# Performance work log

Measured on AMD Instinct MI355X. Metric: run time of the kernel, lower is better.

The kernel has to match this reference:

```python
import jax, jax.numpy as jnp
import numpy as np

N, E, D = 20000, 320000, 256
EPS = 1e-5


def setup_inputs() -> dict:
    key = jax.random.key(0)
    ks = jax.random.split(key, 12)
    s = 1.0 / np.sqrt(D)
    s2 = 1.0 / np.sqrt(2 * D)
    return {
        "node_embeddings": jax.random.normal(ks[0], (N, D), jnp.float32),
        "edge_index": jax.random.randint(ks[1], (2, E), 0, N, jnp.int64),
        "edge_embeddings": jax.random.normal(ks[2], (E, D), jnp.float32),
        # message MLP: Linear(D,D) -> GELU -> Linear(D,D)
        "W1m": jax.random.uniform(ks[3], (D, D), jnp.float32, -s, s),
        "b1m": jnp.zeros((D,), jnp.float32),
        "W2m": jax.random.uniform(ks[4], (D, D), jnp.float32, -s, s),
        "b2m": jnp.zeros((D,), jnp.float32),
        # update MLP: Linear(D,2D) -> GELU -> Linear(2D,D)
        "W1u": jax.random.uniform(ks[5], (D, 2 * D), jnp.float32, -s, s),
        "b1u": jnp.zeros((2 * D,), jnp.float32),
        "W2u": jax.random.uniform(ks[6], (2 * D, D), jnp.float32, -s2, s2),
        "b2u": jnp.zeros((D,), jnp.float32),
        # LayerNorm params
        "gamma": jnp.ones((D,), jnp.float32),
        "beta": jnp.zeros((D,), jnp.float32),
    }


def _layer_norm(x, gamma, beta):
    mu = jnp.mean(x, axis=-1, keepdims=True)
    var = jnp.mean(jnp.square(x - mu), axis=-1, keepdims=True)
    return (x - mu) * jax.lax.rsqrt(var + EPS) * gamma + beta


def reference(node_embeddings, edge_index, edge_embeddings,
              W1m, b1m, W2m, b2m, W1u, b1u, W2u, b2u, gamma, beta):
    src = edge_index[0]
    dst = edge_index[1]
    n = node_embeddings.shape[0]
    # gather + edge add + message MLP (exact erf GELU, as torch default)
    h = node_embeddings[src] + edge_embeddings           # [E, D]
    h = jax.nn.gelu(h @ W1m + b1m, approximate=False)
    messages = h @ W2m + b2m                             # [E, D]
    # scatter-mean aggregation
    agg = jax.ops.segment_sum(messages, dst, num_segments=n)  # [N, D]
    deg = jax.ops.segment_sum(jnp.ones((dst.shape[0], 1), node_embeddings.dtype),
                              dst, num_segments=n)            # [N, 1]
    agg = agg / jnp.maximum(deg, 1.0)
    # update MLP + residual + LayerNorm
    u = jax.nn.gelu(agg @ W1u + b1u, approximate=False) @ W2u + b2u
    return _layer_norm(node_embeddings + u, gamma, beta)
```

## Files before the change

kernel.cpp:

```cpp
#include <hip/hip_runtime.h>
#include <hip/hip_bf16.h>

#define N_NODES 20000
#define N_EDGES 320000
#define EBLK 64
#define NBLK 32

typedef __attribute__((ext_vector_type(8))) short short8;
typedef __attribute__((ext_vector_type(4))) float f32x4;

static __device__ __forceinline__ unsigned short f2bf(float f) {
  __hip_bfloat16 h = __float2bfloat16(f);
  union { __hip_bfloat16 h; unsigned short u; } cv; cv.h = h; return cv.u;
}

static __device__ __forceinline__ float bf2f(unsigned short u) {
  union { unsigned int u; float f; } cv; cv.u = ((unsigned int)u) << 16; return cv.f;
}

static __device__ __forceinline__ unsigned int pk2(float a, float b) {
  return (unsigned int)f2bf(a) | ((unsigned int)f2bf(b) << 16);
}

static __device__ __forceinline__ float gelu_f(float x) {
  float z = x * (2.3022082f + 0.1029432f * x * x);
  z = fminf(fmaxf(z, -30.0f), 30.0f);
  float t = exp2f(z);
  return x * t * __frcp_rn(1.0f + t);
}

#define SWZ(row, byteoff) ((byteoff) ^ (((row) & 7) << 4))
#define SWZU(b) ((b) ^ ((((b) >> 8) & 7) << 4))

__global__ void init_kernel(float4* __restrict__ S4, int4* __restrict__ cnt4,
                            const float* __restrict__ W1m, const float* __restrict__ W2m,
                            const float* __restrict__ W1u, const float* __restrict__ W2u,
                            unsigned short* __restrict__ P1m, unsigned short* __restrict__ P2m,
                            unsigned short* __restrict__ P1u, unsigned short* __restrict__ P2u) {
  const int b = blockIdx.x;
  if (b < 5000) {
    int idx = b * blockDim.x + threadIdx.x;
    S4[idx] = make_float4(0.f, 0.f, 0.f, 0.f);
    if (idx < N_NODES / 4) cnt4[idx] = make_int4(0, 0, 0, 0);
    return;
  }
  int idx = (b - 5000) * blockDim.x + threadIdx.x;
  const float* W; unsigned short* P; int K, Nc, local;
  if (idx < 65536)        { W = W1m; P = P1m; K = 256; Nc = 256; local = idx; }
  else if (idx < 131072)  { W = W2m; P = P2m; K = 256; Nc = 256; local = idx - 65536; }
  else if (idx < 262144)  { W = W1u; P = P1u; K = 256; Nc = 512; local = idx - 131072; }
  else                    { W = W2u; P = P2u; K = 512; Nc = 256; local = idx - 262144; }
  int frag = local >> 9, wi = local & 511;
  int l = wi >> 3, i = wi & 7;
  int kf = K >> 5;
  int cf = frag / kf, t = frag % kf;
  int k = t * 32 + (l >> 4) * 8 + i;
  int n = cf * 16 + (l & 15);
  P[local] = f2bf(W[(size_t)k * Nc + n]);
}

__global__ void hist_kernel(const int* __restrict__ dst, int* __restrict__ cnt) {
  int e = blockIdx.x * blockDim.x + threadIdx.x;
  atomicAdd(&cnt[dst[e]], 1);
}

__global__ __launch_bounds__(1024) void scan_kernel(const int* __restrict__ cnt,
                                                    int* __restrict__ rptr,
                                                    int* __restrict__ cur) {
  __shared__ int sums[1024];
  const int t = threadIdx.x;
  const int base = t * 20;
  int local[20];
  int s = 0;
#pragma unroll
  for (int i = 0; i < 20; ++i) {
    int idx = base + i;
    int v = (idx < N_NODES) ? cnt[idx] : 0;
    local[i] = s;
    s += v;
  }
  int v = s;
  sums[t] = v;
  for (int off = 1; off < 1024; off <<= 1) {
    __syncthreads();
    int o = (t >= off) ? sums[t - off] : 0;
    __syncthreads();
    v += o;
    sums[t] = v;
  }
  int excl = v - s;
#pragma unroll
  for (int i = 0; i < 20; ++i) {
    int idx = base + i;
    if (idx < N_NODES) { int p = excl + local[i]; rptr[idx] = p; cur[idx] = p; }
  }
  if (t == 1023) rptr[N_NODES] = v;
}

__global__ void scatter_kernel(const int* __restrict__ dst, int* __restrict__ cur,
                               int* __restrict__ perm) {
  int e = blockIdx.x * blockDim.x + threadIdx.x;
  int d = dst[e];
  int pos = atomicAdd(&cur[d], 1);
  perm[pos] = e;
}

__global__ __launch_bounds__(256, 4) void nw1_kernel(
    const float* __restrict__ node, const unsigned short* __restrict__ P1m,
    const float* __restrict__ b1m, unsigned short* __restrict__ NW1) {
  __shared__ unsigned short tA[NBLK * 256];
  const int tid = threadIdx.x;
  const int n0 = blockIdx.x * NBLK;
  {
    const int r = tid >> 3;
    const int cs = (tid & 7) * 32;
    const float* np = node + (size_t)(n0 + r) * 256 + cs;
#pragma unroll
    for (int i = 0; i < 4; ++i) {
      float4 a = *(const float4*)(np + i * 8);
      float4 b = *(const float4*)(np + i * 8 + 4);
      uint4 p;
      p.x = pk2(a.x, a.y); p.y = pk2(a.z, a.w);
      p.z = pk2(b.x, b.y); p.w = pk2(b.z, b.w);
      *(uint4*)((char*)tA + SWZ(r, r * 512 + (cs + i * 8) * 2)) = p;
    }
  }
  __syncthreads();
  const int w = tid >> 6, l = tid & 63, lr = l & 15, lh = l >> 4;
  f32x4 acc[2][4];
#pragma unroll
  for (int r4 = 0; r4 < 2; ++r4)
#pragma unroll
    for (int c = 0; c < 4; ++c) acc[r4][c] = f32x4{0.f, 0.f, 0.f, 0.f};
#pragma unroll
  for (int t = 0; t < 8; ++t) {
    const int row0 = lr, row1 = 16 + lr;
    short8 af0 = *(const short8*)((const char*)tA + SWZ(row0, row0 * 512 + t * 64 + lh * 16));
    short8 af1 = *(const short8*)((const char*)tA + SWZ(row1, row1 * 512 + t * 64 + lh * 16));
#pragma unroll
    for (int c = 0; c < 4; ++c) {
      short8 bfr = *(const short8*)(P1m + (size_t)(((w * 4 + c) * 8 + t) * 512 + l * 8));
      acc[0][c] = __builtin_amdgcn_mfma_f32_16x16x32_bf16(af0, bfr, acc[0][c], 0, 0, 0);
      acc[1][c] = __builtin_amdgcn_mfma_f32_16x16x32_bf16(af1, bfr, acc[1][c], 0, 0, 0);
    }
  }
#pragma unroll
  for (int r4 = 0; r4 < 2; ++r4)
#pragma unroll
    for (int c = 0; c < 4; ++c) {
      int col = w * 64 + c * 16 + lr;
      float bb = b1m[col];
#pragma unroll
      for (int j = 0; j < 4; ++j) {
        int row = r4 * 16 + lh * 4 + j;
        NW1[(size_t)(n0 + row) * 256 + col] = f2bf(acc[r4][c][j] + bb);
      }
    }
}

__global__ __launch_bounds__(512, 7) void edge_kernel(
    const float* __restrict__ eemb,
    const int* __restrict__ src, const int* __restrict__ dst,
    const int* __restrict__ perm,
    const unsigned short* __restrict__ P1m, const unsigned short* __restrict__ NW1,
    float* __restrict__ S) {
  __shared__ unsigned short tA[EBLK * 256];
  __shared__ int dstS[EBLK], srcS[EBLK];
  const int tid = threadIdx.x;
  const int e0 = blockIdx.x * EBLK;
  {
    const int r = tid >> 3;
    const int cs = (tid & 7) * 32;
    const int e = perm[e0 + r];
    if ((tid & 7) == 0) { dstS[r] = dst[e]; srcS[r] = src[e]; }
    const float* ep = eemb + (size_t)e * 256 + cs;
#pragma unroll
    for (int i = 0; i < 4; ++i) {
      float4 a = *(const float4*)(ep + i * 8);
      float4 b = *(const float4*)(ep + i * 8 + 4);
      uint4 p;
      p.x = pk2(a.x, a.y); p.y = pk2(a.z, a.w);
      p.z = pk2(b.x, b.y); p.w = pk2(b.z, b.w);
      *(uint4*)((char*)tA + SWZ(r, r * 512 + (cs + i * 8) * 2)) = p;
    }
  }
  __syncthreads();

  const int w = tid >> 6, l = tid & 63;
  const int lr = l & 15, lh = l >> 4;
  const int colbase = w * 32 + lr;

  unsigned short nw0[4][4], nw1[4][4];
#pragma unroll
  for (int r4 = 0; r4 < 4; ++r4)
#pragma unroll
    for (int j = 0; j < 4; ++j) {
      int row = r4 * 16 + lh * 4 + j;
      const unsigned short* nwp = NW1 + (size_t)srcS[row] * 256 + colbase;
      nw0[r4][j] = nwp[0];
      nw1[r4][j] = nwp[16];
    }

  f32x4 acc[4][2];
#pragma unroll
  for (int r4 = 0; r4 < 4; ++r4)
#pragma unroll
    for (int c = 0; c < 2; ++c) acc[r4][c] = f32x4{0.f, 0.f, 0.f, 0.f};
#pragma unroll
  for (int kt = 0; kt < 8; ++kt) {
    short8 af[4];
#pragma unroll
    for (int r4 = 0; r4 < 4; ++r4) {
      int row = r4 * 16 + lr;
      af[r4] = *(const short8*)((const char*)tA + SWZ(row, row * 512 + kt * 64 + lh * 16));
    }
#pragma unroll
    for (int c = 0; c < 2; ++c) {
      short8 bfr = *(const short8*)(P1m + (size_t)(((w * 2 + c) * 8 + kt) * 512 + l * 8));
#pragma unroll
      for (int r4 = 0; r4 < 4; ++r4)
        acc[r4][c] = __builtin_amdgcn_mfma_f32_16x16x32_bf16(af[r4], bfr, acc[r4][c], 0, 0, 0);
    }
  }

#pragma unroll
  for (int r4 = 0; r4 < 4; ++r4)
#pragma unroll
    for (int j = 0; j < 4; ++j) {
      acc[r4][0][j] = gelu_f(acc[r4][0][j] + bf2f(nw0[r4][j]));
      acc[r4][1][j] = gelu_f(acc[r4][1][j] + bf2f(nw1[r4][j]));
    }

  const int dv = dstS[l];
  const int pv = __shfl(dv, (l - 1) & 63);
  const bool bflag = (l == 0) || (dv != pv);
  const unsigned long long mask = __ballot(bflag);
  const int nseg = __popcll(mask);
  int sid[4][4];
#pragma unroll
  for (int r4 = 0; r4 < 4; ++r4)
#pragma unroll
    for (int j = 0; j < 4; ++j) {
      int row = r4 * 16 + lh * 4 + j;
      sid[r4][j] = __popcll(mask & ((2ULL << row) - 1)) - 1;
    }
  unsigned long long rem = mask;
  for (int s = 0; s < nseg; ++s) {
    const int rowf = __builtin_ctzll(rem);
    rem &= rem - 1;
    const int dseg = __shfl(dv, rowf);
    float p0 = 0.f, p1 = 0.f;
#pragma unroll
    for (int r4 = 0; r4 < 4; ++r4)
#pragma unroll
      for (int j = 0; j < 4; ++j) {
        bool m = (sid[r4][j] == s);
        p0 += m ? acc[r4][0][j] : 0.f;
        p1 += m ? acc[r4][1][j] : 0.f;
      }
    p0 += __shfl_xor(p0, 16); p0 += __shfl_xor(p0, 32);
    p1 += __shfl_xor(p1, 16); p1 += __shfl_xor(p1, 32);
    if (lh == 0) {
      float* Sp = S + (size_t)dseg * 256 + colbase;
      atomicAdd(Sp, p0);
      atomicAdd(Sp + 16, p1);
    }
  }
}

__global__ __launch_bounds__(256, 4) void node_kernel(
    const float* __restrict__ node, const float* __restrict__ S, const int* __restrict__ rptr,
    const unsigned short* __restrict__ P2m, const float* __restrict__ b2m,
    const unsigned short* __restrict__ P1u, const float* __restrict__ b1u,
    const unsigned short* __restrict__ P2u, const float* __restrict__ b2u,
    const float* __restrict__ gamma, const float* __restrict__ beta,
    float* __restrict__ out) {
  __shared__ unsigned short tAB[2][NBLK * 256];
  __shared__ unsigned short tH[NBLK * 256];
  __shared__ float fmu[NBLK], frs[NBLK], fflag[NBLK];
  float* tU = (float*)tAB;
  const int tid = threadIdx.x;
  const int n0 = blockIdx.x * NBLK;
  const int r = tid >> 3;
  const int cs = (tid & 7) * 32;
  const int n = n0 + r;
  {
    int dgi = rptr[n + 1] - rptr[n];
    float rec = 1.0f / fmaxf((float)dgi, 1.0f);
    if ((tid & 7) == 0) fflag[r] = (dgi > 0) ? 1.0f : 0.0f;
    const float* sp = S + (size_t)n * 256 + cs;
#pragma unroll
    for (int i = 0; i < 4; ++i) {
      float4 a = *(const float4*)(sp + i * 8);
      float4 b = *(const float4*)(sp + i * 8 + 4);
      uint4 p;
      p.x = pk2(a.x * rec, a.y * rec);
      p.y = pk2(a.z * rec, a.w * rec);
      p.z = pk2(b.x * rec, b.y * rec);
      p.w = pk2(b.z * rec, b.w * rec);
      *(uint4*)((char*)tAB[0] + SWZ(r, r * 512 + (cs + i * 8) * 2)) = p;
    }
  }
  __syncthreads();
  const int w = tid >> 6, l = tid & 63, lr = l & 15, lh = l >> 4;

  {
    f32x4 acc[2][4];
#pragma unroll
    for (int r4 = 0; r4 < 2; ++r4)
#pragma unroll
      for (int c = 0; c < 4; ++c) acc[r4][c] = f32x4{0.f, 0.f, 0.f, 0.f};
#pragma unroll
    for (int t = 0; t < 8; ++t) {
      const int row0 = lr, row1 = 16 + lr;
      short8 af0 = *(const short8*)((const char*)tAB[0] + SWZ(row0, row0 * 512 + t * 64 + lh * 16));
      short8 af1 = *(const short8*)((const char*)tAB[0] + SWZ(row1, row1 * 512 + t * 64 + lh * 16));
#pragma unroll
      for (int c = 0; c < 4; ++c) {
        short8 bfr = *(const short8*)(P2m + (size_t)(((w * 4 + c) * 8 + t) * 512 + l * 8));
        acc[0][c] = __builtin_amdgcn_mfma_f32_16x16x32_bf16(af0, bfr, acc[0][c], 0, 0, 0);
        acc[1][c] = __builtin_amdgcn_mfma_f32_16x16x32_bf16(af1, bfr, acc[1][c], 0, 0, 0);
      }
    }
#pragma unroll
    for (int r4 = 0; r4 < 2; ++r4)
#pragma unroll
      for (int c = 0; c < 4; ++c) {
        int col = w * 64 + c * 16 + lr;
        float bm = b2m[col];
#pragma unroll
        for (int j = 0; j < 4; ++j) {
          int row = r4 * 16 + lh * 4 + j;
          float v = acc[r4][c][j] + fflag[row] * bm;
          *(unsigned short*)((char*)tAB[1] + SWZ(row, row * 512 + col * 2)) = f2bf(v);
        }
      }
  }
  __syncthreads();

  f32x4 acc3[2][4];
#pragma unroll
  for (int c = 0; c < 4; ++c) {
    float bb = b2u[w * 64 + c * 16 + lr];
    acc3[0][c] = f32x4{bb, bb, bb, bb};
    acc3[1][c] = f32x4{bb, bb, bb, bb};
  }
#pragma unroll
  for (int half = 0; half < 2; ++half) {
    {
      f32x4 acc[2][4];
#pragma unroll
      for (int r4 = 0; r4 < 2; ++r4)
#pragma unroll
        for (int c = 0; c < 4; ++c) acc[r4][c] = f32x4{0.f, 0.f, 0.f, 0.f};
#pragma unroll
      for (int t = 0; t < 8; ++t) {
        const int row0 = lr, row1 = 16 + lr;
        short8 af0 = *(const short8*)((const char*)tAB[1] + SWZ(row0, row0 * 512 + t * 64 + lh * 16));
        short8 af1 = *(const short8*)((const char*)tAB[1] + SWZ(row1, row1 * 512 + t * 64 + lh * 16));
#pragma unroll
        for (int c = 0; c < 4; ++c) {
          short8 bfr = *(const short8*)(P1u + (size_t)(((half * 16 + w * 4 + c) * 8 + t) * 512 + l * 8));
          acc[0][c] = __builtin_amdgcn_mfma_f32_16x16x32_bf16(af0, bfr, acc[0][c], 0, 0, 0);
          acc[1][c] = __builtin_amdgcn_mfma_f32_16x16x32_bf16(af1, bfr, acc[1][c], 0, 0, 0);
        }
      }
#pragma unroll
      for (int r4 = 0; r4 < 2; ++r4)
#pragma unroll
        for (int c = 0; c < 4; ++c) {
          int col = w * 64 + c * 16 + lr;
          float b1 = b1u[half * 256 + col];
#pragma unroll
          for (int j = 0; j < 4; ++j) {
            int row = r4 * 16 + lh * 4 + j;
            float v = gelu_f(acc[r4][c][j] + b1);
            *(unsigned short*)((char*)tH + SWZ(row, row * 512 + col * 2)) = f2bf(v);
          }
        }
    }
    __syncthreads();
    {
#pragma unroll
      for (int tt = 0; tt < 8; ++tt) {
        const int row0 = lr, row1 = 16 + lr;
        short8 af0 = *(const short8*)((const char*)tH + SWZ(row0, row0 * 512 + tt * 64 + lh * 16));
        short8 af1 = *(const short8*)((const char*)tH + SWZ(row1, row1 * 512 + tt * 64 + lh * 16));
#pragma unroll
        for (int c = 0; c < 4; ++c) {
          short8 bfr = *(const short8*)(P2u + (size_t)(((w * 4 + c) * 16 + half * 8 + tt) * 512 + l * 8));
          acc3[0][c] = __builtin_amdgcn_mfma_f32_16x16x32_bf16(af0, bfr, acc3[0][c], 0, 0, 0);
          acc3[1][c] = __builtin_amdgcn_mfma_f32_16x16x32_bf16(af1, bfr, acc3[1][c], 0, 0, 0);
        }
      }
    }
    __syncthreads();
  }

#pragma unroll
  for (int r4 = 0; r4 < 2; ++r4)
#pragma unroll
    for (int c = 0; c < 4; ++c) {
      int col = w * 64 + c * 16 + lr;
#pragma unroll
      for (int j = 0; j < 4; ++j) {
        int row = r4 * 16 + lh * 4 + j;
        *(float*)((char*)tU + SWZU(row * 1024 + col * 4)) = acc3[r4][c][j];
      }
    }
  __syncthreads();

  {
    float sum = 0.f, sq = 0.f;
#pragma unroll
    for (int i = 0; i < 8; ++i) {
      int byte = SWZU(r * 1024 + (cs + i * 4) * 4);
      float4 v = *(float4*)((char*)tU + byte);
      const float4 nb = *(const float4*)(node + (size_t)n * 256 + cs + i * 4);
      v.x += nb.x; v.y += nb.y; v.z += nb.z; v.w += nb.w;
      *(float4*)((char*)tU + byte) = v;
      sum += v.x + v.y + v.z + v.w;
      sq += v.x * v.x + v.y * v.y + v.z * v.z + v.w * v.w;
    }
    sum += __shfl_xor(sum, 1); sum += __shfl_xor(sum, 2); sum += __shfl_xor(sum, 4);
    sq  += __shfl_xor(sq, 1);  sq  += __shfl_xor(sq, 2);  sq  += __shfl_xor(sq, 4);
    if ((tid & 7) == 0) {
      float mu = sum * (1.0f / 256.0f);
      fmu[r] = mu;
      frs[r] = rsqrtf(fmaxf(sq * (1.0f / 256.0f) - mu * mu, 0.0f) + 1e-5f);
    }
  }
  __syncthreads();
#pragma unroll
  for (int i = 0; i < 8; ++i) {
    int f4 = i * 256 + tid;
    int row = f4 >> 6;
    int c4 = f4 & 63;
    float4 v = *(float4*)((char*)tU + SWZU(row * 1024 + c4 * 16));
    float mu = fmu[row], rs = frs[row];
    float4 g  = *(const float4*)(gamma + c4 * 4);
    float4 bt = *(const float4*)(beta + c4 * 4);
    float4 o;
    o.x = (v.x - mu) * rs * g.x + bt.x;
    o.y = (v.y - mu) * rs * g.y + bt.y;
    o.z = (v.z - mu) * rs * g.z + bt.z;
    o.w = (v.w - mu) * rs * g.w + bt.w;
    *(float4*)(out + (size_t)(n0 + row) * 256 + c4 * 4) = o;
  }
}

extern "C" void kernel_launch(void* const* d_in, const int* in_sizes, int n_in,
                              void* d_out, int out_size, void* d_ws, size_t ws_size,
                              hipStream_t stream) {
  const float* node = (const float*)d_in[0];
  const int* eidx = (const int*)d_in[1];
  const float* eemb = (const float*)d_in[2];
  const float* W1m = (const float*)d_in[3];
  const float* b1m = (const float*)d_in[4];
  const float* W2m = (const float*)d_in[5];
  const float* b2m = (const float*)d_in[6];
  const float* W1u = (const float*)d_in[7];
  const float* b1u = (const float*)d_in[8];
  const float* W2u = (const float*)d_in[9];
  const float* b2u = (const float*)d_in[10];
  const float* gamma = (const float*)d_in[11];
  const float* beta = (const float*)d_in[12];
  float* out = (float*)d_out;

  char* ws = (char*)d_ws;
  int* cnt  = (int*)ws;
  int* rptr = (int*)(ws + 81920);
  int* cur  = (int*)(ws + 163840);
  int* perm = (int*)(ws + 245760);
  unsigned short* P1m = (unsigned short*)(ws + 1525760);
  unsigned short* P2m = (unsigned short*)(ws + 1656832);
  unsigned short* P1u = (unsigned short*)(ws + 1787904);
  unsigned short* P2u = (unsigned short*)(ws + 2050048);
  unsigned short* NW1 = (unsigned short*)(ws + 2312192);
  const int* src = eidx;
  const int* dst = eidx + N_EDGES;

  init_kernel<<<5000 + 1536, 256, 0, stream>>>((float4*)out, (int4*)cnt,
                                               W1m, W2m, W1u, W2u, P1m, P2m, P1u, P2u);
  hist_kernel<<<N_EDGES / 256, 256, 0, stream>>>(dst, cnt);
  scan_kernel<<<1, 1024, 0, stream>>>(cnt, rptr, cur);
  scatter_kernel<<<N_EDGES / 256, 256, 0, stream>>>(dst, cur, perm);
  nw1_kernel<<<N_NODES / NBLK, 256, 0, stream>>>(node, P1m, b1m, NW1);
  edge_kernel<<<N_EDGES / EBLK, 512, 0, stream>>>(eemb, src, dst, perm, P1m, NW1, out);
  node_kernel<<<N_NODES / NBLK, 256, 0, stream>>>(node, out, rptr, P2m, b2m,
                                                  P1u, b1u, P2u, b2u, gamma, beta, out);
}
```

Before: 314.3 us.

## Stage edge messages in LDS and reduce dst segments with per-column running sums

Replaces the per-wave ballot and shuffle segmented reduction with a different path. GELU outputs are written as bf16 into shared memory, then each thread walks 32 sorted rows for one column, keeping a running sum. Segments that lie entirely inside a thread's row range are written with plain stores, and only boundary segments use atomics. This cuts the serial per-segment shuffle loop and most global atomics, at the cost of two block barriers, an LDS round-trip and bf16 rounding before summation. Launch bounds occupancy is also raised from 7 to 8.

Result: slower. 423.7 us (+34.8%).

```diff
diff --git a/kernel.cpp b/kernel.cpp
--- a/kernel.cpp
+++ b/kernel.cpp
@@ -158,7 +158,7 @@
     }
 }
 
-__global__ __launch_bounds__(512, 7) void edge_kernel(
+__global__ __launch_bounds__(512, 8) void edge_kernel(
     const float* __restrict__ eemb,
     const int* __restrict__ src, const int* __restrict__ dst,
     const int* __restrict__ perm,
@@ -231,40 +231,41 @@
       acc[r4][1][j] = gelu_f(acc[r4][1][j] + bf2f(nw1[r4][j]));
     }
 
-  const int dv = dstS[l];
-  const int pv = __shfl(dv, (l - 1) & 63);
-  const bool bflag = (l == 0) || (dv != pv);
-  const unsigned long long mask = __ballot(bflag);
-  const int nseg = __popcll(mask);
-  int sid[4][4];
+  __syncthreads();
+
 #pragma unroll
   for (int r4 = 0; r4 < 4; ++r4)
 #pragma unroll
-    for (int j = 0; j < 4; ++j) {
-      int row = r4 * 16 + lh * 4 + j;
-      sid[r4][j] = __popcll(mask & ((2ULL << row) - 1)) - 1;
-    }
-  unsigned long long rem = mask;
-  for (int s = 0; s < nseg; ++s) {
-    const int rowf = __builtin_ctzll(rem);
-    rem &= rem - 1;
-    const int dseg = __shfl(dv, rowf);
-    float p0 = 0.f, p1 = 0.f;
-#pragma unroll
-    for (int r4 = 0; r4 < 4; ++r4)
+    for (int c = 0; c < 2; ++c) {
+      int col = w * 32 + c * 16 + lr;
 #pragma unroll
       for (int j = 0; j < 4; ++j) {
-        bool m = (sid[r4][j] == s);
-        p0 += m ? acc[r4][0][j] : 0.f;
-        p1 += m ? acc[r4][1][j] : 0.f;
-      }
-    p0 += __shfl_xor(p0, 16); p0 += __shfl_xor(p0, 32);
-    p1 += __shfl_xor(p1, 16); p1 += __shfl_xor(p1, 32);
-    if (lh == 0) {
-      float* Sp = S + (size_t)dseg * 256 + colbase;
-      atomicAdd(Sp, p0);
-      atomicAdd(Sp + 16, p1);
-    }
+        int row = r4 * 16 + lh * 4 + j;
+        *(unsigned short*)((char*)tA + SWZ(row, row * 512 + col * 2)) = f2bf(acc[r4][c][j]);
+      }
+    }
+  __syncthreads();
+
+  {
+    const int col = tid & 255;
+    const int rbase = (tid >> 8) * 32;
+    float run = 0.f;
+    int cur = dstS[rbase];
+    bool inside = false;
+#pragma unroll 8
+    for (int i = 0; i < 32; ++i) {
+      int row = rbase + i;
+      int d = dstS[row];
+      float v = bf2f(*(const unsigned short*)((const char*)tA + SWZ(row, row * 512 + col * 2)));
+      if (d != cur) {
+        float* gp = S + (size_t)cur * 256 + col;
+        if (inside) *gp = run;
+        else atomicAdd(gp, run);
+        run = 0.f; cur = d; inside = true;
+      }
+      run += v;
+    }
+    atomicAdd(S + (size_t)cur * 256 + col, run);
   }
 }
 
```

## Merge scatter into nw1 launch, use shuffle scan, memset for zeroing

Applied to the files above, without the earlier changes.

Replaces the zero-init part of the init kernel with hipMemsetAsync calls and keeps a separate pack kernel for the weights. The single-block scan now uses wavefront shuffle scans plus a small per-wave sum table instead of a shared-memory Hillis-Steele loop with many barriers. The edge scatter (perm build) is folded into the nw1 kernel as extra blocks, removing one launch and letting the two independent jobs overlap. It also doubles the node kernel's tH shared buffer, which raises LDS use and may reduce occupancy.

New measurement: 313.7 us. Within noise of the previous version (-0.2%).

```diff
diff --git a/kernel.cpp b/kernel.cpp
--- a/kernel.cpp
+++ b/kernel.cpp
@@ -32,19 +32,11 @@
 #define SWZ(row, byteoff) ((byteoff) ^ (((row) & 7) << 4))
 #define SWZU(b) ((b) ^ ((((b) >> 8) & 7) << 4))
 
-__global__ void init_kernel(float4* __restrict__ S4, int4* __restrict__ cnt4,
-                            const float* __restrict__ W1m, const float* __restrict__ W2m,
+__global__ void pack_kernel(const float* __restrict__ W1m, const float* __restrict__ W2m,
                             const float* __restrict__ W1u, const float* __restrict__ W2u,
                             unsigned short* __restrict__ P1m, unsigned short* __restrict__ P2m,
                             unsigned short* __restrict__ P1u, unsigned short* __restrict__ P2u) {
-  const int b = blockIdx.x;
-  if (b < 5000) {
-    int idx = b * blockDim.x + threadIdx.x;
-    S4[idx] = make_float4(0.f, 0.f, 0.f, 0.f);
-    if (idx < N_NODES / 4) cnt4[idx] = make_int4(0, 0, 0, 0);
-    return;
-  }
-  int idx = (b - 5000) * blockDim.x + threadIdx.x;
+  int idx = blockIdx.x * blockDim.x + threadIdx.x;
   const float* W; unsigned short* P; int K, Nc, local;
   if (idx < 65536)        { W = W1m; P = P1m; K = 256; Nc = 256; local = idx; }
   else if (idx < 131072)  { W = W2m; P = P2m; K = 256; Nc = 256; local = idx - 65536; }
@@ -67,8 +59,9 @@
 __global__ __launch_bounds__(1024) void scan_kernel(const int* __restrict__ cnt,
                                                     int* __restrict__ rptr,
                                                     int* __restrict__ cur) {
-  __shared__ int sums[1024];
+  __shared__ int wsum[16];
   const int t = threadIdx.x;
+  const int lane = t & 63, wid = t >> 6;
   const int base = t * 20;
   int local[20];
   int s = 0;
@@ -79,38 +72,49 @@
     local[i] = s;
     s += v;
   }
-  int v = s;
-  sums[t] = v;
-  for (int off = 1; off < 1024; off <<= 1) {
-    __syncthreads();
-    int o = (t >= off) ? sums[t - off] : 0;
-    __syncthreads();
-    v += o;
-    sums[t] = v;
-  }
-  int excl = v - s;
+  int x = s;
+#pragma unroll
+  for (int off = 1; off < 64; off <<= 1) {
+    int v = __shfl_up(x, off);
+    if (lane >= off) x += v;
+  }
+  if (lane == 63) wsum[wid] = x;
+  __syncthreads();
+  if (t < 16) {
+    int y = wsum[t];
+#pragma unroll
+    for (int off = 1; off < 16; off <<= 1) {
+      int v = __shfl_up(y, off);
+      if (t >= off) y += v;
+    }
+    wsum[t] = y;
+  }
+  __syncthreads();
+  const int woff = (wid > 0) ? wsum[wid - 1] : 0;
+  const int incl = x + woff;
+  const int excl = incl - s;
 #pragma unroll
   for (int i = 0; i < 20; ++i) {
     int idx = base + i;
     if (idx < N_NODES) { int p = excl + local[i]; rptr[idx] = p; cur[idx] = p; }
   }
-  if (t == 1023) rptr[N_NODES] = v;
-}
-
-__global__ void scatter_kernel(const int* __restrict__ dst, int* __restrict__ cur,
-                               int* __restrict__ perm) {
-  int e = blockIdx.x * blockDim.x + threadIdx.x;
-  int d = dst[e];
-  int pos = atomicAdd(&cur[d], 1);
-  perm[pos] = e;
-}
-
-__global__ __launch_bounds__(256, 4) void nw1_kernel(
+  if (t == 1023) rptr[N_NODES] = incl;
+}
+
+__global__ __launch_bounds__(256, 4) void scatnw1_kernel(
+    const int* __restrict__ dst, int* __restrict__ cur, int* __restrict__ perm,
     const float* __restrict__ node, const unsigned short* __restrict__ P1m,
     const float* __restrict__ b1m, unsigned short* __restrict__ NW1) {
   __shared__ unsigned short tA[NBLK * 256];
   const int tid = threadIdx.x;
-  const int n0 = blockIdx.x * NBLK;
+  if (blockIdx.x < 1250) {
+    int e = blockIdx.x * 256 + tid;
+    int d = dst[e];
+    int pos = atomicAdd(&cur[d], 1);
+    perm[pos] = e;
+    return;
+  }
+  const int n0 = (blockIdx.x - 1250) * NBLK;
   {
     const int r = tid >> 3;
     const int cs = (tid & 7) * 32;
@@ -276,7 +280,7 @@
     const float* __restrict__ gamma, const float* __restrict__ beta,
     float* __restrict__ out) {
   __shared__ unsigned short tAB[2][NBLK * 256];
-  __shared__ unsigned short tH[NBLK * 256];
+  __shared__ unsigned short tH[NBLK * 512];
   __shared__ float fmu[NBLK], frs[NBLK], fflag[NBLK];
   float* tU = (float*)tAB;
   const int tid = threadIdx.x;
@@ -480,12 +484,12 @@
   const int* src = eidx;
   const int* dst = eidx + N_EDGES;
 
-  init_kernel<<<5000 + 1536, 256, 0, stream>>>((float4*)out, (int4*)cnt,
-                                               W1m, W2m, W1u, W2u, P1m, P2m, P1u, P2u);
+  hipMemsetAsync(out, 0, (size_t)N_NODES * 256 * 4, stream);
+  hipMemsetAsync(cnt, 0, (size_t)N_NODES * 4, stream);
+  pack_kernel<<<1536, 256, 0, stream>>>(W1m, W2m, W1u, W2u, P1m, P2m, P1u, P2u);
   hist_kernel<<<N_EDGES / 256, 256, 0, stream>>>(dst, cnt);
   scan_kernel<<<1, 1024, 0, stream>>>(cnt, rptr, cur);
-  scatter_kernel<<<N_EDGES / 256, 256, 0, stream>>>(dst, cur, perm);
-  nw1_kernel<<<N_NODES / NBLK, 256, 0, stream>>>(node, P1m, b1m, NW1);
+  scatnw1_kernel<<<1250 + 625, 256, 0, stream>>>(dst, cur, perm, node, P1m, b1m, NW1);
   edge_kernel<<<N_EDGES / EBLK, 512, 0, stream>>>(eemb, src, dst, perm, P1m, NW1, out);
   node_kernel<<<N_NODES / NBLK, 256, 0, stream>>>(node, out, rptr, P2m, b2m,
                                                   P1u, b1u, P2u, b2u, gamma, beta, out);
```
